# Kernel optimization log

Hardware: AMD Instinct MI355X
Metric: run time of the kernel (lower is better)

The kernel has to match this reference:

```python
import jax, jax.numpy as jnp
import numpy as np
from jax import lax

B, T = 512, 128
V, D, H, MLP, C = 50000, 300, 512, 1024, 3


def setup_inputs() -> dict:
    key = jax.random.key(0)
    ks = jax.random.split(key, 12)
    s = 0.02
    x = jax.random.randint(ks[0], (B, T), 0, V, dtype=jnp.int64)
    lengths = jax.random.randint(ks[1], (B,), 1, T + 1, dtype=jnp.int64)
    return {
        "x": x,
        "lengths": lengths,
        "E": jax.random.normal(ks[2], (V, D), jnp.float32) * s,
        "W_ih": jax.random.normal(ks[3], (H, D), jnp.float32) * s,
        "b_ih": jnp.zeros((H,), jnp.float32),
        "W_hh": jax.random.normal(ks[4], (H, H), jnp.float32) * s,
        "b_hh": jnp.zeros((H,), jnp.float32),
        "l0_w": jax.random.normal(ks[5], (MLP, H), jnp.float32) * s,
        "l0_b": jnp.zeros((MLP,), jnp.float32),
        "l1_w": jax.random.normal(ks[6], (C, MLP), jnp.float32) * s,
        "l1_b": jnp.zeros((C,), jnp.float32),
    }


def reference(x, lengths, E, W_ih, b_ih, W_hh, b_hh, l0_w, l0_b, l1_w, l1_b):
    # Original pops tokens from the end of each sample, right-aligned by length:
    # at step t the active samples (l >= T - t) consume token x[i, T-1-t],
    # i.e. each sequence is processed in reverse token order; hidden state of
    # inactive samples stays untouched (zeros until the sample becomes active).
    Bn, Tn = x.shape
    Hn = W_hh.shape[0]
    toks = x[:, ::-1].T                                    # [T, B] token at step t
    idxs = jnp.arange(Tn)[::-1]                            # index T-1-t at step t
    active = idxs[:, None] < lengths[None, :]              # [T, B]

    def step(h, inp):
        tok, m = inp
        emb = E[tok]                                       # [B, D] gather
        h_next = jnp.tanh(emb @ W_ih.T + b_ih + h @ W_hh.T + b_hh)
        h = jnp.where(m[:, None], h_next, h)               # scatter-back for active rows
        return h, None

    h0 = jnp.zeros((Bn, Hn), E.dtype)
    h, _ = lax.scan(step, h0, (toks, active))
    # eval mode: dropout(p=0.5, training=False) is identity
    a = jax.nn.relu(h @ l0_w.T + l0_b)
    logits = jax.nn.relu(a @ l1_w.T + l1_b)
    return jax.nn.log_softmax(logits, axis=-1)
```

## Files before the change

kernel.cpp:

```cpp
#include <hip/hip_runtime.h>
#include <hip/hip_bf16.h>
#include <cstdint>

#define BB 512
#define TT 128
#define VV 50000
#define DD 300
#define HH 512
#define MLPD 1024
#define CC 3

typedef __bf16 bf16x8 __attribute__((ext_vector_type(8)));
typedef float  f32x4  __attribute__((ext_vector_type(4)));
typedef float  f32x2  __attribute__((ext_vector_type(2)));
typedef int    v8i    __attribute__((ext_vector_type(8)));
typedef int    v4i    __attribute__((ext_vector_type(4)));

struct alignas(8)  bf4 { __bf16 x, y, z, w; };

__device__ __forceinline__ f32x2 tanh16pk(float x0, float x1) {
    f32x2 t;
    t.x = __builtin_amdgcn_fmed3f(x0, -0.7f, 0.7f);
    t.y = __builtin_amdgcn_fmed3f(x1, -0.7f, 0.7f);
    f32x2 u = t * t;
    f32x2 inner = u * 2.1333333f - 5.3333333f;
    return (t * u) * inner + t * 16.0f;
}

#define SCALE_H 0x7B7B7B7B
#define SCALE_W 0x7C7C7C7C

__global__ __launch_bounds__(256) void k_prep(
    const float* __restrict__ Whh, unsigned char* __restrict__ out8,
    const float* __restrict__ Wihf, __bf16* __restrict__ outih,
    const float* __restrict__ l0w, __bf16* __restrict__ outl0)
{
    if (blockIdx.x < 32) {
        const int T = blockIdx.x * 256 + threadIdx.x;
        const int lane = T & 63;
        const int kch = (T >> 6) & 3;
        const int ct  = (T >> 8) & 3;
        const int w   = (T >> 10) & 7;
        const int n = lane & 15, q = lane >> 4;
        const int c  = w * 64 + ct * 16 + n;
        const int k0 = kch * 128 + q * 32;
        const float* src = Whh + c * HH + k0;
        unsigned int wd[8];
        #pragma unroll
        for (int i = 0; i < 8; ++i) {
            float4 v = *(const float4*)(src + i * 4);
            unsigned int t0 = __builtin_amdgcn_cvt_pk_fp8_f32(v.x * 8.f, v.y * 8.f, 0, false);
            t0 = __builtin_amdgcn_cvt_pk_fp8_f32(v.z * 8.f, v.w * 8.f, t0, true);
            wd[i] = t0;
        }
        *(uint4*)(out8 + (size_t)T * 32)      = make_uint4(wd[0], wd[1], wd[2], wd[3]);
        *(uint4*)(out8 + (size_t)T * 32 + 16) = make_uint4(wd[4], wd[5], wd[6], wd[7]);
    } else if (blockIdx.x < 112) {
        const int U = (blockIdx.x - 32) * 256 + threadIdx.x;
        const int lane = U & 63;
        const int rest = U >> 6;
        const int kc = rest % 10;
        const int g  = rest / 10;
        const int c = g * 16 + (lane & 15);
        const int k = kc * 32 + (lane >> 4) * 8;
        bf16x8 o;
        #pragma unroll
        for (int j = 0; j < 8; ++j) {
            const int kk = k + j;
            o[j] = (__bf16)((kk < DD) ? Wihf[c * DD + kk] : 0.f);
        }
        *(bf16x8*)(outih + (size_t)U * 8) = o;
    } else {
        const int F = (blockIdx.x - 112) * 256 + threadIdx.x;
        const int lane = F & 63;
        const int kc = (F >> 6) & 15;
        const int nt = F >> 10;
        const int c = nt * 16 + (lane & 15);
        const int k = kc * 32 + (lane >> 4) * 8;
        const float* src = l0w + (size_t)c * HH + k;
        float4 v0 = *(const float4*)src;
        float4 v1 = *(const float4*)(src + 4);
        bf16x8 o;
        o[0]=(__bf16)v0.x; o[1]=(__bf16)v0.y; o[2]=(__bf16)v0.z; o[3]=(__bf16)v0.w;
        o[4]=(__bf16)v1.x; o[5]=(__bf16)v1.y; o[6]=(__bf16)v1.z; o[7]=(__bf16)v1.w;
        *(bf16x8*)(outl0 + (size_t)F * 8) = o;
    }
}

__global__ __launch_bounds__(256, 1) void k_proj(
    const int* __restrict__ x, const int* __restrict__ lengths,
    const float* __restrict__ E, const __bf16* __restrict__ Wih,
    const float* __restrict__ b_ih, const float* __restrict__ b_hh,
    __bf16* __restrict__ P_c)
{
    __shared__ __bf16 Afs[4][10 * 64 * 8];
    __shared__ float bias_s[HH];

    const int tq  = blockIdx.x;
    const int i0  = blockIdx.y * 64;
    const int wg0 = blockIdx.y * 4;
    const int tid = threadIdx.x;
    const int wv = tid >> 6, lane = tid & 63;
    const int np = lane & 15;

    bias_s[tid]       = b_ih[tid]       + b_hh[tid];
    bias_s[tid + 256] = b_ih[tid + 256] + b_hh[tid + 256];
    __syncthreads();

    bf16x8 Af[4][10];
    {
        const int k0a = lane * 4;
        const int cha = k0a >> 5, ga = (k0a >> 3) & 3;
        const int k0b = 256 + lane * 4;
        const int chb = k0b >> 5, gb = (k0b >> 3) & 3;
        for (int tt = 0; tt < 4; ++tt) {
            const int thr = TT - 1 - (tq * 4 + tt);
            #pragma unroll 4
            for (int rl = 0; rl < 16; ++rl) {
                const int gr = i0 + wv * 16 + rl;
                const bool act = thr < lengths[gr];
                float4 v0 = make_float4(0.f, 0.f, 0.f, 0.f);
                float4 v1 = make_float4(0.f, 0.f, 0.f, 0.f);
                if (act) {
                    const float* erow = E + (size_t)x[gr * TT + thr] * DD;
                    v0 = *(const float4*)(erow + k0a);
                    if (lane < 11) v1 = *(const float4*)(erow + k0b);
                }
                bf4 p0 = {(__bf16)v0.x, (__bf16)v0.y, (__bf16)v0.z, (__bf16)v0.w};
                *(bf4*)(&Afs[wv][((cha * 64) + rl + 16 * ga) * 8 + (k0a & 7)]) = p0;
                if (lane < 16) {
                    bf4 p1 = {(__bf16)v1.x, (__bf16)v1.y, (__bf16)v1.z, (__bf16)v1.w};
                    *(bf4*)(&Afs[wv][((chb * 64) + rl + 16 * gb) * 8 + (k0b & 7)]) = p1;
                }
            }
            #pragma unroll
            for (int kc = 0; kc < 10; ++kc)
                Af[tt][kc] = *(const bf16x8*)(&Afs[wv][(kc * 64 + lane) * 8]);
        }
    }

    for (int ntq = 0; ntq < 8; ++ntq) {
        bf4 pkbuf[4][4];
        #pragma unroll
        for (int j = 0; j < 4; ++j) {
            const int nt = ntq * 4 + j;
            const __bf16* bbase = Wih + ((size_t)(nt * 10) * 64 + lane) * 8;
            bf16x8 Bf[10];
            #pragma unroll
            for (int kc = 0; kc < 10; ++kc)
                Bf[kc] = *(const bf16x8*)(bbase + (size_t)kc * 512);

            f32x4 acc[4] = {};
            #pragma unroll
            for (int kc = 0; kc < 10; ++kc) {
                acc[0] = __builtin_amdgcn_mfma_f32_16x16x32_bf16(Af[0][kc], Bf[kc], acc[0], 0, 0, 0);
                acc[1] = __builtin_amdgcn_mfma_f32_16x16x32_bf16(Af[1][kc], Bf[kc], acc[1], 0, 0, 0);
                acc[2] = __builtin_amdgcn_mfma_f32_16x16x32_bf16(Af[2][kc], Bf[kc], acc[2], 0, 0, 0);
                acc[3] = __builtin_amdgcn_mfma_f32_16x16x32_bf16(Af[3][kc], Bf[kc], acc[3], 0, 0, 0);
            }

            const float bias = bias_s[nt * 16 + np];
            #pragma unroll
            for (int tt = 0; tt < 4; ++tt)
                pkbuf[tt][j] = bf4{(__bf16)(acc[tt][0] + bias), (__bf16)(acc[tt][1] + bias),
                                   (__bf16)(acc[tt][2] + bias), (__bf16)(acc[tt][3] + bias)};
        }
        #pragma unroll
        for (int tt = 0; tt < 4; ++tt) {
            const int t = tq * 4 + tt;
            unsigned char* dst = (unsigned char*)P_c
                + ((size_t)((t * 32 + wg0 + wv) * 8 + ntq)) * 2048 + (size_t)lane * 32;
            *(uint4*)(dst)      = *(uint4*)(&pkbuf[tt][0]);
            *(uint4*)(dst + 16) = *(uint4*)(&pkbuf[tt][2]);
        }
    }
}

#define LKH 520

__global__ __launch_bounds__(512, 2) void k_rnn(
    const int* __restrict__ lengths, const unsigned char* __restrict__ Wb8,
    const __bf16* __restrict__ P_c, const __bf16* __restrict__ l0wf,
    const float* __restrict__ l0_b, const float* __restrict__ l1_w,
    const float* __restrict__ l1_b, float* __restrict__ out)
{
    __shared__ unsigned char smem[50944];
    unsigned char (*Hs8)[8192] = (unsigned char (*)[8192])smem;
    __bf16* As   = (__bf16*)(smem + 16384);
    float*  l1s  = (float*)(smem + 33024);
    float*  l0bs = (float*)(smem + 45312);
    float (*red)[16][3] = (float (*)[16][3])(smem + 49408);

    const int tid = threadIdx.x;
    const int wg  = blockIdx.x;
    const int r0  = wg * 16;
    const int w    = tid >> 6;
    const int lane = tid & 63;
    const int n = lane & 15, q = lane >> 4;

    for (int i = tid * 16; i < 16384; i += 512 * 16)
        *(uint4*)(&smem[i]) = make_uint4(0u, 0u, 0u, 0u);

    for (int i = tid; i < 3 * MLPD; i += 512) l1s[i] = l1_w[i];
    for (int i = tid; i < MLPD; i += 512)     l0bs[i] = l0_b[i];

    const int len_n = lengths[r0 + n];
    const int tact  = TT - len_n;
    int ml = len_n;
    #pragma unroll
    for (int off = 1; off <= 8; off <<= 1) {
        int o = __shfl_xor(ml, off, 64);
        ml = ml > o ? ml : o;
    }
    const int t0 = (TT - ml) & ~1;

    v8i Wv[4][4];
    #pragma unroll
    for (int ct = 0; ct < 4; ++ct)
        #pragma unroll
        for (int kch = 0; kch < 4; ++kch)
            Wv[ct][kch] = *(const v8i*)(Wb8 + ((size_t)(((w * 4 + ct) * 4 + kch) * 64 + lane)) * 32);

    const int wsw = ((n >> 2) & 1) << 4;
    int waddr[4];
    #pragma unroll
    for (int ct = 0; ct < 4; ++ct)
        waddr[ct] = ((((w >> 1) * 64 + n + 16 * ((2 * w + (ct >> 1)) & 3)) * 32
                  + (ct & 1) * 16 + q * 4)) ^ wsw;

    const int rsw = ((lane >> 2) & 1) << 4;

    const size_t pstep = (size_t)32 * 8 * 2048;
    const unsigned char* pptr = (const unsigned char*)P_c
                              + ((size_t)(wg * 8 + w)) * 2048 + (size_t)lane * 32
                              + (size_t)t0 * pstep;

    __syncthreads();

    bf16x8 plo = *(const bf16x8*)(pptr);
    bf16x8 phi = *(const bf16x8*)(pptr + 16);
    pptr += pstep;

    auto step = [&](int t, const unsigned char* rbuf, unsigned char* wbuf) {
        bf16x8 nlo = *(const bf16x8*)(pptr);
        bf16x8 nhi = *(const bf16x8*)(pptr + 16);
        pptr += pstep;

        v8i hf[4];
        #pragma unroll
        for (int kch = 0; kch < 4; ++kch) {
            const unsigned char* rb = rbuf + (kch * 64 + lane) * 32;
            v4i lo = *(const v4i*)(rb + rsw);
            v4i hi = *(const v4i*)(rb + (16 ^ rsw));
            hf[kch] = __builtin_shufflevector(lo, hi, 0, 1, 2, 3, 4, 5, 6, 7);
        }

        const bool act = (t >= tact);

        {
            f32x4 a0, a1;
            #pragma unroll
            for (int r = 0; r < 4; ++r) { a0[r] = (float)plo[r]; a1[r] = (float)plo[4 + r]; }
            a0 = __builtin_amdgcn_mfma_scale_f32_16x16x128_f8f6f4(Wv[0][0], hf[0], a0, 0, 0, 0, SCALE_W, 0, SCALE_H);
            a1 = __builtin_amdgcn_mfma_scale_f32_16x16x128_f8f6f4(Wv[1][0], hf[0], a1, 0, 0, 0, SCALE_W, 0, SCALE_H);
            a0 = __builtin_amdgcn_mfma_scale_f32_16x16x128_f8f6f4(Wv[0][1], hf[1], a0, 0, 0, 0, SCALE_W, 0, SCALE_H);
            a1 = __builtin_amdgcn_mfma_scale_f32_16x16x128_f8f6f4(Wv[1][1], hf[1], a1, 0, 0, 0, SCALE_W, 0, SCALE_H);
            a0 = __builtin_amdgcn_mfma_scale_f32_16x16x128_f8f6f4(Wv[0][2], hf[2], a0, 0, 0, 0, SCALE_W, 0, SCALE_H);
            a1 = __builtin_amdgcn_mfma_scale_f32_16x16x128_f8f6f4(Wv[1][2], hf[2], a1, 0, 0, 0, SCALE_W, 0, SCALE_H);
            a0 = __builtin_amdgcn_mfma_scale_f32_16x16x128_f8f6f4(Wv[0][3], hf[3], a0, 0, 0, 0, SCALE_W, 0, SCALE_H);
            a1 = __builtin_amdgcn_mfma_scale_f32_16x16x128_f8f6f4(Wv[1][3], hf[3], a1, 0, 0, 0, SCALE_W, 0, SCALE_H);

            f32x2 s00 = tanh16pk(a0[0], a0[1]);
            f32x2 s01 = tanh16pk(a0[2], a0[3]);
            f32x2 s10 = tanh16pk(a1[0], a1[1]);
            f32x2 s11 = tanh16pk(a1[2], a1[3]);
            unsigned p0 = __builtin_amdgcn_cvt_pk_fp8_f32(s00.x, s00.y, 0u, false);
            p0 = __builtin_amdgcn_cvt_pk_fp8_f32(s01.x, s01.y, p0, true);
            unsigned p1 = __builtin_amdgcn_cvt_pk_fp8_f32(s10.x, s10.y, 0u, false);
            p1 = __builtin_amdgcn_cvt_pk_fp8_f32(s11.x, s11.y, p1, true);
            *(unsigned int*)(&wbuf[waddr[0]]) = act ? p0 : 0u;
            *(unsigned int*)(&wbuf[waddr[1]]) = act ? p1 : 0u;
        }

        {
            f32x4 a2, a3;
            #pragma unroll
            for (int r = 0; r < 4; ++r) { a2[r] = (float)phi[r]; a3[r] = (float)phi[4 + r]; }
            a2 = __builtin_amdgcn_mfma_scale_f32_16x16x128_f8f6f4(Wv[2][0], hf[0], a2, 0, 0, 0, SCALE_W, 0, SCALE_H);
            a3 = __builtin_amdgcn_mfma_scale_f32_16x16x128_f8f6f4(Wv[3][0], hf[0], a3, 0, 0, 0, SCALE_W, 0, SCALE_H);
            a2 = __builtin_amdgcn_mfma_scale_f32_16x16x128_f8f6f4(Wv[2][1], hf[1], a2, 0, 0, 0, SCALE_W, 0, SCALE_H);
            a3 = __builtin_amdgcn_mfma_scale_f32_16x16x128_f8f6f4(Wv[3][1], hf[1], a3, 0, 0, 0, SCALE_W, 0, SCALE_H);
            a2 = __builtin_amdgcn_mfma_scale_f32_16x16x128_f8f6f4(Wv[2][2], hf[2], a2, 0, 0, 0, SCALE_W, 0, SCALE_H);
            a3 = __builtin_amdgcn_mfma_scale_f32_16x16x128_f8f6f4(Wv[3][2], hf[2], a3, 0, 0, 0, SCALE_W, 0, SCALE_H);
            a2 = __builtin_amdgcn_mfma_scale_f32_16x16x128_f8f6f4(Wv[2][3], hf[3], a2, 0, 0, 0, SCALE_W, 0, SCALE_H);
            a3 = __builtin_amdgcn_mfma_scale_f32_16x16x128_f8f6f4(Wv[3][3], hf[3], a3, 0, 0, 0, SCALE_W, 0, SCALE_H);

            f32x2 s20 = tanh16pk(a2[0], a2[1]);
            f32x2 s21 = tanh16pk(a2[2], a2[3]);
            f32x2 s30 = tanh16pk(a3[0], a3[1]);
            f32x2 s31 = tanh16pk(a3[2], a3[3]);
            unsigned p2 = __builtin_amdgcn_cvt_pk_fp8_f32(s20.x, s20.y, 0u, false);
            p2 = __builtin_amdgcn_cvt_pk_fp8_f32(s21.x, s21.y, p2, true);
            unsigned p3 = __builtin_amdgcn_cvt_pk_fp8_f32(s30.x, s30.y, 0u, false);
            p3 = __builtin_amdgcn_cvt_pk_fp8_f32(s31.x, s31.y, p3, true);
            *(unsigned int*)(&wbuf[waddr[2]]) = act ? p2 : 0u;
            *(unsigned int*)(&wbuf[waddr[3]]) = act ? p3 : 0u;
        }

        plo = nlo; phi = nhi;
        __syncthreads();
    };

    for (int t = t0; t < TT; t += 2) {
        step(t,     Hs8[0], Hs8[1]);
        step(t + 1, Hs8[1], Hs8[0]);
    }

    {
        const int half   = tid & 1;
        const int lane_t = (tid >> 1) & 63;
        const int kch    = tid >> 7;
        const int m  = lane_t & 15, qq = lane_t >> 4;
        const int cb = kch * 128 + qq * 32 + half * 16;
        const int sw2 = ((lane_t >> 2) & 1) << 4;
        uint4 wv4 = *(const uint4*)(&Hs8[0][(kch * 64 + lane_t) * 32 + ((half * 16) ^ sw2)]);
        unsigned int ws4[4] = {wv4.x, wv4.y, wv4.z, wv4.w};
        bf16x8 o0, o1;
        #pragma unroll
        for (int wd = 0; wd < 4; ++wd) {
            float f0 = __builtin_amdgcn_cvt_f32_fp8(ws4[wd], 0) * 0.0625f;
            float f1 = __builtin_amdgcn_cvt_f32_fp8(ws4[wd], 1) * 0.0625f;
            float f2 = __builtin_amdgcn_cvt_f32_fp8(ws4[wd], 2) * 0.0625f;
            float f3 = __builtin_amdgcn_cvt_f32_fp8(ws4[wd], 3) * 0.0625f;
            if (wd < 2) {
                o0[wd * 4 + 0] = (__bf16)f0; o0[wd * 4 + 1] = (__bf16)f1;
                o0[wd * 4 + 2] = (__bf16)f2; o0[wd * 4 + 3] = (__bf16)f3;
            } else {
                o1[(wd - 2) * 4 + 0] = (__bf16)f0; o1[(wd - 2) * 4 + 1] = (__bf16)f1;
                o1[(wd - 2) * 4 + 2] = (__bf16)f2; o1[(wd - 2) * 4 + 3] = (__bf16)f3;
            }
        }
        *(bf16x8*)(&As[m * LKH + cb])     = o0;
        *(bf16x8*)(&As[m * LKH + cb + 8]) = o1;
    }
    __syncthreads();

    float pl[4][3] = {};
    for (int j = 0; j < 8; ++j) {
        const int ntile = w * 8 + j;
        const __bf16* bb = l0wf + ((size_t)(ntile * 16) * 64 + lane) * 8;
        bf16x8 Bf[16];
        #pragma unroll
        for (int kc = 0; kc < 16; ++kc)
            Bf[kc] = *(const bf16x8*)(bb + (size_t)kc * 512);

        f32x4 acc = {};
        #pragma unroll
        for (int kc = 0; kc < 16; ++kc) {
            bf16x8 a = *(const bf16x8*)(&As[n * LKH + kc * 32 + q * 8]);
            acc = __builtin_amdgcn_mfma_f32_16x16x32_bf16(a, Bf[kc], acc, 0, 0, 0);
        }

        const int col = ntile * 16 + n;
        const float b0 = l0bs[col];
        const float w0 = l1s[col], w1 = l1s[MLPD + col], w2 = l1s[2 * MLPD + col];
        #pragma unroll
        for (int r = 0; r < 4; ++r) {
            const float av = fmaxf(acc[r] + b0, 0.f);
            pl[r][0] = fmaf(av, w0, pl[r][0]);
            pl[r][1] = fmaf(av, w1, pl[r][1]);
            pl[r][2] = fmaf(av, w2, pl[r][2]);
        }
    }

    #pragma unroll
    for (int off = 1; off <= 8; off <<= 1)
        #pragma unroll
        for (int r = 0; r < 4; ++r)
            #pragma unroll
            for (int c = 0; c < 3; ++c)
                pl[r][c] += __shfl_xor(pl[r][c], off, 64);

    if (n == 0)
        #pragma unroll
        for (int r = 0; r < 4; ++r)
            #pragma unroll
            for (int c = 0; c < 3; ++c)
                red[w][q * 4 + r][c] = pl[r][c];
    __syncthreads();

    if (tid < 16) {
        const int row = tid;
        float l[3];
        #pragma unroll
        for (int c = 0; c < 3; ++c) {
            float s = l1_b[c];
            #pragma unroll
            for (int ww = 0; ww < 8; ++ww) s += red[ww][row][c];
            l[c] = fmaxf(s, 0.f);
        }
        float m = fmaxf(l[0], fmaxf(l[1], l[2]));
        float sum = expf(l[0] - m) + expf(l[1] - m) + expf(l[2] - m);
        float ls = m + logf(sum);
        out[(r0 + row) * CC + 0] = l[0] - ls;
        out[(r0 + row) * CC + 1] = l[1] - ls;
        out[(r0 + row) * CC + 2] = l[2] - ls;
    }
}

extern "C" void kernel_launch(void* const* d_in, const int* in_sizes, int n_in,
                              void* d_out, int out_size, void* d_ws, size_t ws_size,
                              hipStream_t stream) {
    const int*   x    = (const int*)  d_in[0];
    const int*   len  = (const int*)  d_in[1];
    const float* E    = (const float*)d_in[2];
    const float* W_ih = (const float*)d_in[3];
    const float* b_ih = (const float*)d_in[4];
    const float* W_hh = (const float*)d_in[5];
    const float* b_hh = (const float*)d_in[6];
    const float* l0_w = (const float*)d_in[7];
    const float* l0_b = (const float*)d_in[8];
    const float* l1_w = (const float*)d_in[9];
    const float* l1_b = (const float*)d_in[10];
    float* out = (float*)d_out;

    char* ws = (char*)d_ws;
    unsigned char* Wb8 = (unsigned char*)ws;
    __bf16* Wih   = (__bf16*)(ws + 524288);
    __bf16* l0wf  = (__bf16*)(ws + 1048576);
    __bf16* P_c   = (__bf16*)(ws + 4194304);

    k_prep<<<368, 256, 0, stream>>>(W_hh, Wb8, W_ih, Wih, l0_w, l0wf);
    dim3 g1(32, 8);
    k_proj<<<g1, 256, 0, stream>>>(x, len, E, Wih, b_ih, b_hh, P_c);
    k_rnn<<<32, 512, 0, stream>>>(len, Wb8, P_c, l0wf, l0_b, l1_w, l1_b, out);
}
```

Baseline: 323.0 us.

## Replace per-step block barrier with LDS flag-based wave sync and 4-deep ring

Each RNN time step ended in a __syncthreads. That is now replaced by per-wave progress flags in shared memory, and the hidden state moves to a 4-slot LDS ring. Each wave spins only on the flags of the two waves that produced the K-chunk it needs next. Waves start on different chunks to stagger their waits, so MFMAs on ready chunks can begin before all waves finish. In exchange the code adds busy-wait polling, more LDS use (which may affect the 2-blocks-per-CU occupancy), and memory-ordering risk from relying on lgkmcnt plus volatile flags.

```diff
diff --git a/kernel.cpp b/kernel.cpp
--- a/kernel.cpp
+++ b/kernel.cpp
@@ -184,12 +184,15 @@
     const float* __restrict__ l0_b, const float* __restrict__ l1_w,
     const float* __restrict__ l1_b, float* __restrict__ out)
 {
-    __shared__ unsigned char smem[50944];
-    unsigned char (*Hs8)[8192] = (unsigned char (*)[8192])smem;
-    __bf16* As   = (__bf16*)(smem + 16384);
-    float*  l1s  = (float*)(smem + 33024);
-    float*  l0bs = (float*)(smem + 45312);
-    float (*red)[16][3] = (float (*)[16][3])(smem + 49408);
+    __shared__ unsigned char smem[67360];
+    unsigned char* ring = smem;
+    int*    flg  = (int*)(smem + 32768);
+    __bf16* As   = (__bf16*)(smem + 32832);
+    float*  l1s  = (float*)(smem + 49472);
+    float*  l0bs = (float*)(smem + 61760);
+    float (*red)[16][3] = (float (*)[16][3])(smem + 65856);
+
+    volatile int* vflg = (volatile int*)flg;
 
     const int tid = threadIdx.x;
     const int wg  = blockIdx.x;
@@ -197,8 +200,9 @@
     const int w    = tid >> 6;
     const int lane = tid & 63;
     const int n = lane & 15, q = lane >> 4;
-
-    for (int i = tid * 16; i < 16384; i += 512 * 16)
+    const int pr = w >> 1;
+
+    for (int i = tid * 16; i < 32768; i += 512 * 16)
         *(uint4*)(&smem[i]) = make_uint4(0u, 0u, 0u, 0u);
 
     for (int i = tid; i < 3 * MLPD; i += 512) l1s[i] = l1_w[i];
@@ -212,7 +216,9 @@
         int o = __shfl_xor(ml, off, 64);
         ml = ml > o ? ml : o;
     }
-    const int t0 = (TT - ml) & ~1;
+    const int t0 = TT - ml;
+
+    if (tid < 8) flg[tid] = t0 - 1;
 
     v8i Wv[4][4];
     #pragma unroll
@@ -241,89 +247,77 @@
     bf16x8 phi = *(const bf16x8*)(pptr + 16);
     pptr += pstep;
 
-    auto step = [&](int t, const unsigned char* rbuf, unsigned char* wbuf) {
+    for (int t = t0; t < TT; ++t) {
+        const unsigned char* rbuf = ring + (size_t)((t + 3) & 3) * 8192;
+        unsigned char*       wbuf = ring + (size_t)(t & 3) * 8192;
+
         bf16x8 nlo = *(const bf16x8*)(pptr);
         bf16x8 nhi = *(const bf16x8*)(pptr + 16);
         pptr += pstep;
 
-        v8i hf[4];
-        #pragma unroll
-        for (int kch = 0; kch < 4; ++kch) {
-            const unsigned char* rb = rbuf + (kch * 64 + lane) * 32;
+        const bool act = (t >= tact);
+        const int tm1 = t - 1;
+
+        f32x4 a0, a1, a2, a3;
+        #pragma unroll
+        for (int r = 0; r < 4; ++r) {
+            a0[r] = (float)plo[r]; a1[r] = (float)plo[4 + r];
+            a2[r] = (float)phi[r]; a3[r] = (float)phi[4 + r];
+        }
+
+        #pragma unroll
+        for (int g = 0; g < 4; ++g) {
+            const int kk = (pr + g) & 3;
+            while (vflg[2 * kk] < tm1 || vflg[2 * kk + 1] < tm1) {}
+            asm volatile("" ::: "memory");
+            const unsigned char* rb = rbuf + (kk * 64 + lane) * 32;
             v4i lo = *(const v4i*)(rb + rsw);
             v4i hi = *(const v4i*)(rb + (16 ^ rsw));
-            hf[kch] = __builtin_shufflevector(lo, hi, 0, 1, 2, 3, 4, 5, 6, 7);
-        }
-
-        const bool act = (t >= tact);
-
-        {
-            f32x4 a0, a1;
-            #pragma unroll
-            for (int r = 0; r < 4; ++r) { a0[r] = (float)plo[r]; a1[r] = (float)plo[4 + r]; }
-            a0 = __builtin_amdgcn_mfma_scale_f32_16x16x128_f8f6f4(Wv[0][0], hf[0], a0, 0, 0, 0, SCALE_W, 0, SCALE_H);
-            a1 = __builtin_amdgcn_mfma_scale_f32_16x16x128_f8f6f4(Wv[1][0], hf[0], a1, 0, 0, 0, SCALE_W, 0, SCALE_H);
-            a0 = __builtin_amdgcn_mfma_scale_f32_16x16x128_f8f6f4(Wv[0][1], hf[1], a0, 0, 0, 0, SCALE_W, 0, SCALE_H);
-            a1 = __builtin_amdgcn_mfma_scale_f32_16x16x128_f8f6f4(Wv[1][1], hf[1], a1, 0, 0, 0, SCALE_W, 0, SCALE_H);
-            a0 = __builtin_amdgcn_mfma_scale_f32_16x16x128_f8f6f4(Wv[0][2], hf[2], a0, 0, 0, 0, SCALE_W, 0, SCALE_H);
-            a1 = __builtin_amdgcn_mfma_scale_f32_16x16x128_f8f6f4(Wv[1][2], hf[2], a1, 0, 0, 0, SCALE_W, 0, SCALE_H);
-            a0 = __builtin_amdgcn_mfma_scale_f32_16x16x128_f8f6f4(Wv[0][3], hf[3], a0, 0, 0, 0, SCALE_W, 0, SCALE_H);
-            a1 = __builtin_amdgcn_mfma_scale_f32_16x16x128_f8f6f4(Wv[1][3], hf[3], a1, 0, 0, 0, SCALE_W, 0, SCALE_H);
-
-            f32x2 s00 = tanh16pk(a0[0], a0[1]);
-            f32x2 s01 = tanh16pk(a0[2], a0[3]);
-            f32x2 s10 = tanh16pk(a1[0], a1[1]);
-            f32x2 s11 = tanh16pk(a1[2], a1[3]);
-            unsigned p0 = __builtin_amdgcn_cvt_pk_fp8_f32(s00.x, s00.y, 0u, false);
-            p0 = __builtin_amdgcn_cvt_pk_fp8_f32(s01.x, s01.y, p0, true);
-            unsigned p1 = __builtin_amdgcn_cvt_pk_fp8_f32(s10.x, s10.y, 0u, false);
-            p1 = __builtin_amdgcn_cvt_pk_fp8_f32(s11.x, s11.y, p1, true);
-            *(unsigned int*)(&wbuf[waddr[0]]) = act ? p0 : 0u;
-            *(unsigned int*)(&wbuf[waddr[1]]) = act ? p1 : 0u;
-        }
-
-        {
-            f32x4 a2, a3;
-            #pragma unroll
-            for (int r = 0; r < 4; ++r) { a2[r] = (float)phi[r]; a3[r] = (float)phi[4 + r]; }
-            a2 = __builtin_amdgcn_mfma_scale_f32_16x16x128_f8f6f4(Wv[2][0], hf[0], a2, 0, 0, 0, SCALE_W, 0, SCALE_H);
-            a3 = __builtin_amdgcn_mfma_scale_f32_16x16x128_f8f6f4(Wv[3][0], hf[0], a3, 0, 0, 0, SCALE_W, 0, SCALE_H);
-            a2 = __builtin_amdgcn_mfma_scale_f32_16x16x128_f8f6f4(Wv[2][1], hf[1], a2, 0, 0, 0, SCALE_W, 0, SCALE_H);
-            a3 = __builtin_amdgcn_mfma_scale_f32_16x16x128_f8f6f4(Wv[3][1], hf[1], a3, 0, 0, 0, SCALE_W, 0, SCALE_H);
-            a2 = __builtin_amdgcn_mfma_scale_f32_16x16x128_f8f6f4(Wv[2][2], hf[2], a2, 0, 0, 0, SCALE_W, 0, SCALE_H);
-            a3 = __builtin_amdgcn_mfma_scale_f32_16x16x128_f8f6f4(Wv[3][2], hf[2], a3, 0, 0, 0, SCALE_W, 0, SCALE_H);
-            a2 = __builtin_amdgcn_mfma_scale_f32_16x16x128_f8f6f4(Wv[2][3], hf[3], a2, 0, 0, 0, SCALE_W, 0, SCALE_H);
-            a3 = __builtin_amdgcn_mfma_scale_f32_16x16x128_f8f6f4(Wv[3][3], hf[3], a3, 0, 0, 0, SCALE_W, 0, SCALE_H);
-
-            f32x2 s20 = tanh16pk(a2[0], a2[1]);
-            f32x2 s21 = tanh16pk(a2[2], a2[3]);
-            f32x2 s30 = tanh16pk(a3[0], a3[1]);
-            f32x2 s31 = tanh16pk(a3[2], a3[3]);
-            unsigned p2 = __builtin_amdgcn_cvt_pk_fp8_f32(s20.x, s20.y, 0u, false);
-            p2 = __builtin_amdgcn_cvt_pk_fp8_f32(s21.x, s21.y, p2, true);
-            unsigned p3 = __builtin_amdgcn_cvt_pk_fp8_f32(s30.x, s30.y, 0u, false);
-            p3 = __builtin_amdgcn_cvt_pk_fp8_f32(s31.x, s31.y, p3, true);
-            *(unsigned int*)(&wbuf[waddr[2]]) = act ? p2 : 0u;
-            *(unsigned int*)(&wbuf[waddr[3]]) = act ? p3 : 0u;
-        }
+            v8i hfk = __builtin_shufflevector(lo, hi, 0, 1, 2, 3, 4, 5, 6, 7);
+            a0 = __builtin_amdgcn_mfma_scale_f32_16x16x128_f8f6f4(Wv[0][kk], hfk, a0, 0, 0, 0, SCALE_W, 0, SCALE_H);
+            a1 = __builtin_amdgcn_mfma_scale_f32_16x16x128_f8f6f4(Wv[1][kk], hfk, a1, 0, 0, 0, SCALE_W, 0, SCALE_H);
+            a2 = __builtin_amdgcn_mfma_scale_f32_16x16x128_f8f6f4(Wv[2][kk], hfk, a2, 0, 0, 0, SCALE_W, 0, SCALE_H);
+            a3 = __builtin_amdgcn_mfma_scale_f32_16x16x128_f8f6f4(Wv[3][kk], hfk, a3, 0, 0, 0, SCALE_W, 0, SCALE_H);
+        }
+
+        f32x2 s00 = tanh16pk(a0[0], a0[1]);
+        f32x2 s01 = tanh16pk(a0[2], a0[3]);
+        f32x2 s10 = tanh16pk(a1[0], a1[1]);
+        f32x2 s11 = tanh16pk(a1[2], a1[3]);
+        f32x2 s20 = tanh16pk(a2[0], a2[1]);
+        f32x2 s21 = tanh16pk(a2[2], a2[3]);
+        f32x2 s30 = tanh16pk(a3[0], a3[1]);
+        f32x2 s31 = tanh16pk(a3[2], a3[3]);
+        unsigned p0 = __builtin_amdgcn_cvt_pk_fp8_f32(s00.x, s00.y, 0u, false);
+        p0 = __builtin_amdgcn_cvt_pk_fp8_f32(s01.x, s01.y, p0, true);
+        unsigned p1 = __builtin_amdgcn_cvt_pk_fp8_f32(s10.x, s10.y, 0u, false);
+        p1 = __builtin_amdgcn_cvt_pk_fp8_f32(s11.x, s11.y, p1, true);
+        unsigned p2 = __builtin_amdgcn_cvt_pk_fp8_f32(s20.x, s20.y, 0u, false);
+        p2 = __builtin_amdgcn_cvt_pk_fp8_f32(s21.x, s21.y, p2, true);
+        unsigned p3 = __builtin_amdgcn_cvt_pk_fp8_f32(s30.x, s30.y, 0u, false);
+        p3 = __builtin_amdgcn_cvt_pk_fp8_f32(s31.x, s31.y, p3, true);
+        *(unsigned int*)(&wbuf[waddr[0]]) = act ? p0 : 0u;
+        *(unsigned int*)(&wbuf[waddr[1]]) = act ? p1 : 0u;
+        *(unsigned int*)(&wbuf[waddr[2]]) = act ? p2 : 0u;
+        *(unsigned int*)(&wbuf[waddr[3]]) = act ? p3 : 0u;
+
+        asm volatile("s_waitcnt lgkmcnt(0)" ::: "memory");
+        vflg[w] = t;
 
         plo = nlo; phi = nhi;
-        __syncthreads();
-    };
-
-    for (int t = t0; t < TT; t += 2) {
-        step(t,     Hs8[0], Hs8[1]);
-        step(t + 1, Hs8[1], Hs8[0]);
-    }
+    }
+
+    __syncthreads();
 
     {
+        const unsigned char* hfin = ring + (size_t)((TT - 1) & 3) * 8192;
         const int half   = tid & 1;
         const int lane_t = (tid >> 1) & 63;
         const int kch    = tid >> 7;
         const int m  = lane_t & 15, qq = lane_t >> 4;
         const int cb = kch * 128 + qq * 32 + half * 16;
         const int sw2 = ((lane_t >> 2) & 1) << 4;
-        uint4 wv4 = *(const uint4*)(&Hs8[0][(kch * 64 + lane_t) * 32 + ((half * 16) ^ sw2)]);
+        uint4 wv4 = *(const uint4*)(&hfin[(kch * 64 + lane_t) * 32 + ((half * 16) ^ sw2)]);
         unsigned int ws4[4] = {wv4.x, wv4.y, wv4.z, wv4.w};
         bf16x8 o0, o1;
         #pragma unroll
```

Result: slower. 1.180 ms (+265.2%).

## Sort samples by length to skip inactive projection tiles and shorten RNN loops

Applied to the files above, without the earlier changes.

Adds a single-block rank sort of sequence lengths that produces a permutation and a per-64-row maximum length. The input projection gathers rows through the permutation, and whole blocks return early when every sample in the tile is inactive at those timesteps. The projection grid is doubled with two timesteps per block and occupancy 2 to keep the skip finer grained. The RNN kernel reads the permuted rows, so each 16-row group has similar lengths and can start later, and outputs are scattered back to their original rows. The cost is an extra kernel launch plus indirect loads.

```diff
diff --git a/kernel.cpp b/kernel.cpp
--- a/kernel.cpp
+++ b/kernel.cpp
@@ -29,6 +29,24 @@
 
 #define SCALE_H 0x7B7B7B7B
 #define SCALE_W 0x7C7C7C7C
+
+__global__ __launch_bounds__(512) void k_sort(
+    const int* __restrict__ lengths, int* __restrict__ perm,
+    int* __restrict__ tileMax)
+{
+    __shared__ int ls[BB];
+    const int i = threadIdx.x;
+    const int li = lengths[i];
+    ls[i] = li;
+    __syncthreads();
+    int rank = 0;
+    for (int j = 0; j < BB; ++j) {
+        const int lj = ls[j];
+        rank += (lj > li) || (lj == li && j < i);
+    }
+    perm[rank] = i;
+    if ((rank & 63) == 0) tileMax[rank >> 6] = li;
+}
 
 __global__ __launch_bounds__(256) void k_prep(
     const float* __restrict__ Whh, unsigned char* __restrict__ out8,
@@ -87,12 +105,15 @@
     }
 }
 
-__global__ __launch_bounds__(256, 1) void k_proj(
+__global__ __launch_bounds__(256, 2) void k_proj(
     const int* __restrict__ x, const int* __restrict__ lengths,
     const float* __restrict__ E, const __bf16* __restrict__ Wih,
     const float* __restrict__ b_ih, const float* __restrict__ b_hh,
-    __bf16* __restrict__ P_c)
+    __bf16* __restrict__ P_c, const int* __restrict__ perm,
+    const int* __restrict__ tileMax)
 {
+    if (tileMax[blockIdx.y] + 2 * (int)blockIdx.x < 127) return;
+
     __shared__ __bf16 Afs[4][10 * 64 * 8];
     __shared__ float bias_s[HH];
 
@@ -107,22 +128,23 @@
     bias_s[tid + 256] = b_ih[tid + 256] + b_hh[tid + 256];
     __syncthreads();
 
-    bf16x8 Af[4][10];
+    bf16x8 Af[2][10];
     {
         const int k0a = lane * 4;
         const int cha = k0a >> 5, ga = (k0a >> 3) & 3;
         const int k0b = 256 + lane * 4;
         const int chb = k0b >> 5, gb = (k0b >> 3) & 3;
-        for (int tt = 0; tt < 4; ++tt) {
-            const int thr = TT - 1 - (tq * 4 + tt);
+        for (int tt = 0; tt < 2; ++tt) {
+            const int thr = TT - 1 - (tq * 2 + tt);
             #pragma unroll 4
             for (int rl = 0; rl < 16; ++rl) {
                 const int gr = i0 + wv * 16 + rl;
-                const bool act = thr < lengths[gr];
+                const int pg = perm[gr];
+                const bool act = thr < lengths[pg];
                 float4 v0 = make_float4(0.f, 0.f, 0.f, 0.f);
                 float4 v1 = make_float4(0.f, 0.f, 0.f, 0.f);
                 if (act) {
-                    const float* erow = E + (size_t)x[gr * TT + thr] * DD;
+                    const float* erow = E + (size_t)x[pg * TT + thr] * DD;
                     v0 = *(const float4*)(erow + k0a);
                     if (lane < 11) v1 = *(const float4*)(erow + k0b);
                 }
@@ -140,7 +162,7 @@
     }
 
     for (int ntq = 0; ntq < 8; ++ntq) {
-        bf4 pkbuf[4][4];
+        bf4 pkbuf[2][4];
         #pragma unroll
         for (int j = 0; j < 4; ++j) {
             const int nt = ntq * 4 + j;
@@ -150,24 +172,22 @@
             for (int kc = 0; kc < 10; ++kc)
                 Bf[kc] = *(const bf16x8*)(bbase + (size_t)kc * 512);
 
-            f32x4 acc[4] = {};
+            f32x4 acc[2] = {};
             #pragma unroll
             for (int kc = 0; kc < 10; ++kc) {
                 acc[0] = __builtin_amdgcn_mfma_f32_16x16x32_bf16(Af[0][kc], Bf[kc], acc[0], 0, 0, 0);
                 acc[1] = __builtin_amdgcn_mfma_f32_16x16x32_bf16(Af[1][kc], Bf[kc], acc[1], 0, 0, 0);
-                acc[2] = __builtin_amdgcn_mfma_f32_16x16x32_bf16(Af[2][kc], Bf[kc], acc[2], 0, 0, 0);
-                acc[3] = __builtin_amdgcn_mfma_f32_16x16x32_bf16(Af[3][kc], Bf[kc], acc[3], 0, 0, 0);
             }
 
             const float bias = bias_s[nt * 16 + np];
             #pragma unroll
-            for (int tt = 0; tt < 4; ++tt)
+            for (int tt = 0; tt < 2; ++tt)
                 pkbuf[tt][j] = bf4{(__bf16)(acc[tt][0] + bias), (__bf16)(acc[tt][1] + bias),
                                    (__bf16)(acc[tt][2] + bias), (__bf16)(acc[tt][3] + bias)};
         }
         #pragma unroll
-        for (int tt = 0; tt < 4; ++tt) {
-            const int t = tq * 4 + tt;
+        for (int tt = 0; tt < 2; ++tt) {
+            const int t = tq * 2 + tt;
             unsigned char* dst = (unsigned char*)P_c
                 + ((size_t)((t * 32 + wg0 + wv) * 8 + ntq)) * 2048 + (size_t)lane * 32;
             *(uint4*)(dst)      = *(uint4*)(&pkbuf[tt][0]);
@@ -182,7 +202,8 @@
     const int* __restrict__ lengths, const unsigned char* __restrict__ Wb8,
     const __bf16* __restrict__ P_c, const __bf16* __restrict__ l0wf,
     const float* __restrict__ l0_b, const float* __restrict__ l1_w,
-    const float* __restrict__ l1_b, float* __restrict__ out)
+    const float* __restrict__ l1_b, float* __restrict__ out,
+    const int* __restrict__ perm)
 {
     __shared__ unsigned char smem[50944];
     unsigned char (*Hs8)[8192] = (unsigned char (*)[8192])smem;
@@ -204,7 +225,7 @@
     for (int i = tid; i < 3 * MLPD; i += 512) l1s[i] = l1_w[i];
     for (int i = tid; i < MLPD; i += 512)     l0bs[i] = l0_b[i];
 
-    const int len_n = lengths[r0 + n];
+    const int len_n = lengths[perm[r0 + n]];
     const int tact  = TT - len_n;
     int ml = len_n;
     #pragma unroll
@@ -391,6 +412,7 @@
 
     if (tid < 16) {
         const int row = tid;
+        const int orow = perm[r0 + row];
         float l[3];
         #pragma unroll
         for (int c = 0; c < 3; ++c) {
@@ -402,9 +424,9 @@
         float m = fmaxf(l[0], fmaxf(l[1], l[2]));
         float sum = expf(l[0] - m) + expf(l[1] - m) + expf(l[2] - m);
         float ls = m + logf(sum);
-        out[(r0 + row) * CC + 0] = l[0] - ls;
-        out[(r0 + row) * CC + 1] = l[1] - ls;
-        out[(r0 + row) * CC + 2] = l[2] - ls;
+        out[orow * CC + 0] = l[0] - ls;
+        out[orow * CC + 1] = l[1] - ls;
+        out[orow * CC + 2] = l[2] - ls;
     }
 }
 
@@ -428,10 +450,13 @@
     unsigned char* Wb8 = (unsigned char*)ws;
     __bf16* Wih   = (__bf16*)(ws + 524288);
     __bf16* l0wf  = (__bf16*)(ws + 1048576);
+    int* permW    = (int*)(ws + 2097152);
+    int* tileMaxW = (int*)(ws + 2097152 + 2048);
     __bf16* P_c   = (__bf16*)(ws + 4194304);
 
     k_prep<<<368, 256, 0, stream>>>(W_hh, Wb8, W_ih, Wih, l0_w, l0wf);
-    dim3 g1(32, 8);
-    k_proj<<<g1, 256, 0, stream>>>(x, len, E, Wih, b_ih, b_hh, P_c);
-    k_rnn<<<32, 512, 0, stream>>>(len, Wb8, P_c, l0wf, l0_b, l1_w, l1_b, out);
-}
+    k_sort<<<1, 512, 0, stream>>>(len, permW, tileMaxW);
+    dim3 g1(64, 8);
+    k_proj<<<g1, 256, 0, stream>>>(x, len, E, Wih, b_ih, b_hh, P_c, permW, tileMaxW);
+    k_rnn<<<32, 512, 0, stream>>>(len, Wb8, P_c, l0wf, l0_b, l1_w, l1_b, out, permW);
+}
```

New measurement: 314.5 us. 1.03x faster.

## Halve RNN block to 4 waves with 8 column tiles each; split projection over more blocks

Applied to the files above, without the earlier changes.

The recurrent kernel now runs 256 threads (4 waves) per block instead of 8 waves. Each wave holds twice as many W_hh fp8 fragments in registers and issues 8 independent MFMA chains per k-chunk, so fewer waves meet at each per-step barrier and each wave has more instruction-level parallelism. The projection kernel processes 2 timesteps per block over a 64x8 grid, with launch bounds raised to 2 blocks per CU for more parallelism. The cost is much higher register pressure in k_rnn, which could spill, plus halved wave-level parallelism in the serial loop and the MLP epilogue.

```diff
diff --git a/kernel.cpp b/kernel.cpp
--- a/kernel.cpp
+++ b/kernel.cpp
@@ -87,7 +87,7 @@
     }
 }
 
-__global__ __launch_bounds__(256, 1) void k_proj(
+__global__ __launch_bounds__(256, 2) void k_proj(
     const int* __restrict__ x, const int* __restrict__ lengths,
     const float* __restrict__ E, const __bf16* __restrict__ Wih,
     const float* __restrict__ b_ih, const float* __restrict__ b_hh,
@@ -107,14 +107,14 @@
     bias_s[tid + 256] = b_ih[tid + 256] + b_hh[tid + 256];
     __syncthreads();
 
-    bf16x8 Af[4][10];
+    bf16x8 Af[2][10];
     {
         const int k0a = lane * 4;
         const int cha = k0a >> 5, ga = (k0a >> 3) & 3;
         const int k0b = 256 + lane * 4;
         const int chb = k0b >> 5, gb = (k0b >> 3) & 3;
-        for (int tt = 0; tt < 4; ++tt) {
-            const int thr = TT - 1 - (tq * 4 + tt);
+        for (int tt = 0; tt < 2; ++tt) {
+            const int thr = TT - 1 - (tq * 2 + tt);
             #pragma unroll 4
             for (int rl = 0; rl < 16; ++rl) {
                 const int gr = i0 + wv * 16 + rl;
@@ -140,7 +140,7 @@
     }
 
     for (int ntq = 0; ntq < 8; ++ntq) {
-        bf4 pkbuf[4][4];
+        bf4 pkbuf[2][4];
         #pragma unroll
         for (int j = 0; j < 4; ++j) {
             const int nt = ntq * 4 + j;
@@ -150,24 +150,22 @@
             for (int kc = 0; kc < 10; ++kc)
                 Bf[kc] = *(const bf16x8*)(bbase + (size_t)kc * 512);
 
-            f32x4 acc[4] = {};
+            f32x4 acc[2] = {};
             #pragma unroll
             for (int kc = 0; kc < 10; ++kc) {
                 acc[0] = __builtin_amdgcn_mfma_f32_16x16x32_bf16(Af[0][kc], Bf[kc], acc[0], 0, 0, 0);
                 acc[1] = __builtin_amdgcn_mfma_f32_16x16x32_bf16(Af[1][kc], Bf[kc], acc[1], 0, 0, 0);
-                acc[2] = __builtin_amdgcn_mfma_f32_16x16x32_bf16(Af[2][kc], Bf[kc], acc[2], 0, 0, 0);
-                acc[3] = __builtin_amdgcn_mfma_f32_16x16x32_bf16(Af[3][kc], Bf[kc], acc[3], 0, 0, 0);
             }
 
             const float bias = bias_s[nt * 16 + np];
             #pragma unroll
-            for (int tt = 0; tt < 4; ++tt)
+            for (int tt = 0; tt < 2; ++tt)
                 pkbuf[tt][j] = bf4{(__bf16)(acc[tt][0] + bias), (__bf16)(acc[tt][1] + bias),
                                    (__bf16)(acc[tt][2] + bias), (__bf16)(acc[tt][3] + bias)};
         }
         #pragma unroll
-        for (int tt = 0; tt < 4; ++tt) {
-            const int t = tq * 4 + tt;
+        for (int tt = 0; tt < 2; ++tt) {
+            const int t = tq * 2 + tt;
             unsigned char* dst = (unsigned char*)P_c
                 + ((size_t)((t * 32 + wg0 + wv) * 8 + ntq)) * 2048 + (size_t)lane * 32;
             *(uint4*)(dst)      = *(uint4*)(&pkbuf[tt][0]);
@@ -178,7 +176,7 @@
 
 #define LKH 520
 
-__global__ __launch_bounds__(512, 2) void k_rnn(
+__global__ __launch_bounds__(256, 1) void k_rnn(
     const int* __restrict__ lengths, const unsigned char* __restrict__ Wb8,
     const __bf16* __restrict__ P_c, const __bf16* __restrict__ l0wf,
     const float* __restrict__ l0_b, const float* __restrict__ l1_w,
@@ -198,11 +196,11 @@
     const int lane = tid & 63;
     const int n = lane & 15, q = lane >> 4;
 
-    for (int i = tid * 16; i < 16384; i += 512 * 16)
+    for (int i = tid * 16; i < 16384; i += 256 * 16)
         *(uint4*)(&smem[i]) = make_uint4(0u, 0u, 0u, 0u);
 
-    for (int i = tid; i < 3 * MLPD; i += 512) l1s[i] = l1_w[i];
-    for (int i = tid; i < MLPD; i += 512)     l0bs[i] = l0_b[i];
+    for (int i = tid; i < 3 * MLPD; i += 256) l1s[i] = l1_w[i];
+    for (int i = tid; i < MLPD; i += 256)     l0bs[i] = l0_b[i];
 
     const int len_n = lengths[r0 + n];
     const int tact  = TT - len_n;
@@ -214,36 +212,39 @@
     }
     const int t0 = (TT - ml) & ~1;
 
-    v8i Wv[4][4];
+    v8i Wv[8][4];
     #pragma unroll
-    for (int ct = 0; ct < 4; ++ct)
+    for (int j = 0; j < 8; ++j)
         #pragma unroll
         for (int kch = 0; kch < 4; ++kch)
-            Wv[ct][kch] = *(const v8i*)(Wb8 + ((size_t)(((w * 4 + ct) * 4 + kch) * 64 + lane)) * 32);
+            Wv[j][kch] = *(const v8i*)(Wb8 + ((size_t)(((w * 8 + j) * 4 + kch) * 64 + lane)) * 32);
 
     const int wsw = ((n >> 2) & 1) << 4;
-    int waddr[4];
+    int waddr[8];
     #pragma unroll
-    for (int ct = 0; ct < 4; ++ct)
-        waddr[ct] = ((((w >> 1) * 64 + n + 16 * ((2 * w + (ct >> 1)) & 3)) * 32
-                  + (ct & 1) * 16 + q * 4)) ^ wsw;
+    for (int j = 0; j < 8; ++j)
+        waddr[j] = ((w * 64 + n + 16 * (j >> 1)) * 32 + (j & 1) * 16 + q * 4) ^ wsw;
 
     const int rsw = ((lane >> 2) & 1) << 4;
 
     const size_t pstep = (size_t)32 * 8 * 2048;
     const unsigned char* pptr = (const unsigned char*)P_c
-                              + ((size_t)(wg * 8 + w)) * 2048 + (size_t)lane * 32
+                              + ((size_t)(wg * 8 + 2 * w)) * 2048 + (size_t)lane * 32
                               + (size_t)t0 * pstep;
 
     __syncthreads();
 
-    bf16x8 plo = *(const bf16x8*)(pptr);
-    bf16x8 phi = *(const bf16x8*)(pptr + 16);
+    bf16x8 p0lo = *(const bf16x8*)(pptr);
+    bf16x8 p0hi = *(const bf16x8*)(pptr + 16);
+    bf16x8 p1lo = *(const bf16x8*)(pptr + 2048);
+    bf16x8 p1hi = *(const bf16x8*)(pptr + 2064);
     pptr += pstep;
 
     auto step = [&](int t, const unsigned char* rbuf, unsigned char* wbuf) {
-        bf16x8 nlo = *(const bf16x8*)(pptr);
-        bf16x8 nhi = *(const bf16x8*)(pptr + 16);
+        bf16x8 n0lo = *(const bf16x8*)(pptr);
+        bf16x8 n0hi = *(const bf16x8*)(pptr + 16);
+        bf16x8 n1lo = *(const bf16x8*)(pptr + 2048);
+        bf16x8 n1hi = *(const bf16x8*)(pptr + 2064);
         pptr += pstep;
 
         v8i hf[4];
@@ -257,57 +258,37 @@
 
         const bool act = (t >= tact);
 
-        {
-            f32x4 a0, a1;
-            #pragma unroll
-            for (int r = 0; r < 4; ++r) { a0[r] = (float)plo[r]; a1[r] = (float)plo[4 + r]; }
-            a0 = __builtin_amdgcn_mfma_scale_f32_16x16x128_f8f6f4(Wv[0][0], hf[0], a0, 0, 0, 0, SCALE_W, 0, SCALE_H);
-            a1 = __builtin_amdgcn_mfma_scale_f32_16x16x128_f8f6f4(Wv[1][0], hf[0], a1, 0, 0, 0, SCALE_W, 0, SCALE_H);
-            a0 = __builtin_amdgcn_mfma_scale_f32_16x16x128_f8f6f4(Wv[0][1], hf[1], a0, 0, 0, 0, SCALE_W, 0, SCALE_H);
-            a1 = __builtin_amdgcn_mfma_scale_f32_16x16x128_f8f6f4(Wv[1][1], hf[1], a1, 0, 0, 0, SCALE_W, 0, SCALE_H);
-            a0 = __builtin_amdgcn_mfma_scale_f32_16x16x128_f8f6f4(Wv[0][2], hf[2], a0, 0, 0, 0, SCALE_W, 0, SCALE_H);
-            a1 = __builtin_amdgcn_mfma_scale_f32_16x16x128_f8f6f4(Wv[1][2], hf[2], a1, 0, 0, 0, SCALE_W, 0, SCALE_H);
-            a0 = __builtin_amdgcn_mfma_scale_f32_16x16x128_f8f6f4(Wv[0][3], hf[3], a0, 0, 0, 0, SCALE_W, 0, SCALE_H);
-            a1 = __builtin_amdgcn_mfma_scale_f32_16x16x128_f8f6f4(Wv[1][3], hf[3], a1, 0, 0, 0, SCALE_W, 0, SCALE_H);
-
-            f32x2 s00 = tanh16pk(a0[0], a0[1]);
-            f32x2 s01 = tanh16pk(a0[2], a0[3]);
-            f32x2 s10 = tanh16pk(a1[0], a1[1]);
-            f32x2 s11 = tanh16pk(a1[2], a1[3]);
-            unsigned p0 = __builtin_amdgcn_cvt_pk_fp8_f32(s00.x, s00.y, 0u, false);
-            p0 = __builtin_amdgcn_cvt_pk_fp8_f32(s01.x, s01.y, p0, true);
-            unsigned p1 = __builtin_amdgcn_cvt_pk_fp8_f32(s10.x, s10.y, 0u, false);
-            p1 = __builtin_amdgcn_cvt_pk_fp8_f32(s11.x, s11.y, p1, true);
-            *(unsigned int*)(&wbuf[waddr[0]]) = act ? p0 : 0u;
-            *(unsigned int*)(&wbuf[waddr[1]]) = act ? p1 : 0u;
-        }
-
-        {
-            f32x4 a2, a3;
-            #pragma unroll
-            for (int r = 0; r < 4; ++r) { a2[r] = (float)phi[r]; a3[r] = (float)phi[4 + r]; }
-            a2 = __builtin_amdgcn_mfma_scale_f32_16x16x128_f8f6f4(Wv[2][0], hf[0], a2, 0, 0, 0, SCALE_W, 0, SCALE_H);
-            a3 = __builtin_amdgcn_mfma_scale_f32_16x16x128_f8f6f4(Wv[3][0], hf[0], a3, 0, 0, 0, SCALE_W, 0, SCALE_H);
-            a2 = __builtin_amdgcn_mfma_scale_f32_16x16x128_f8f6f4(Wv[2][1], hf[1], a2, 0, 0, 0, SCALE_W, 0, SCALE_H);
-            a3 = __builtin_amdgcn_mfma_scale_f32_16x16x128_f8f6f4(Wv[3][1], hf[1], a3, 0, 0, 0, SCALE_W, 0, SCALE_H);
-            a2 = __builtin_amdgcn_mfma_scale_f32_16x16x128_f8f6f4(Wv[2][2], hf[2], a2, 0, 0, 0, SCALE_W, 0, SCALE_H);
-            a3 = __builtin_amdgcn_mfma_scale_f32_16x16x128_f8f6f4(Wv[3][2], hf[2], a3, 0, 0, 0, SCALE_W, 0, SCALE_H);
-            a2 = __builtin_amdgcn_mfma_scale_f32_16x16x128_f8f6f4(Wv[2][3], hf[3], a2, 0, 0, 0, SCALE_W, 0, SCALE_H);
-            a3 = __builtin_amdgcn_mfma_scale_f32_16x16x128_f8f6f4(Wv[3][3], hf[3], a3, 0, 0, 0, SCALE_W, 0, SCALE_H);
-
-            f32x2 s20 = tanh16pk(a2[0], a2[1]);
-            f32x2 s21 = tanh16pk(a2[2], a2[3]);
-            f32x2 s30 = tanh16pk(a3[0], a3[1]);
-            f32x2 s31 = tanh16pk(a3[2], a3[3]);
-            unsigned p2 = __builtin_amdgcn_cvt_pk_fp8_f32(s20.x, s20.y, 0u, false);
-            p2 = __builtin_amdgcn_cvt_pk_fp8_f32(s21.x, s21.y, p2, true);
-            unsigned p3 = __builtin_amdgcn_cvt_pk_fp8_f32(s30.x, s30.y, 0u, false);
-            p3 = __builtin_amdgcn_cvt_pk_fp8_f32(s31.x, s31.y, p3, true);
-            *(unsigned int*)(&wbuf[waddr[2]]) = act ? p2 : 0u;
-            *(unsigned int*)(&wbuf[waddr[3]]) = act ? p3 : 0u;
-        }
-
-        plo = nlo; phi = nhi;
+        f32x4 a[8];
+        #pragma unroll
+        for (int r = 0; r < 4; ++r) {
+            a[0][r] = (float)p0lo[r];     a[1][r] = (float)p0lo[4 + r];
+            a[2][r] = (float)p0hi[r];     a[3][r] = (float)p0hi[4 + r];
+            a[4][r] = (float)p1lo[r];     a[5][r] = (float)p1lo[4 + r];
+            a[6][r] = (float)p1hi[r];     a[7][r] = (float)p1hi[4 + r];
+        }
+
+        #pragma unroll
+        for (int kch = 0; kch < 4; ++kch) {
+            a[0] = __builtin_amdgcn_mfma_scale_f32_16x16x128_f8f6f4(Wv[0][kch], hf[kch], a[0], 0, 0, 0, SCALE_W, 0, SCALE_H);
+            a[1] = __builtin_amdgcn_mfma_scale_f32_16x16x128_f8f6f4(Wv[1][kch], hf[kch], a[1], 0, 0, 0, SCALE_W, 0, SCALE_H);
+            a[2] = __builtin_amdgcn_mfma_scale_f32_16x16x128_f8f6f4(Wv[2][kch], hf[kch], a[2], 0, 0, 0, SCALE_W, 0, SCALE_H);
+            a[3] = __builtin_amdgcn_mfma_scale_f32_16x16x128_f8f6f4(Wv[3][kch], hf[kch], a[3], 0, 0, 0, SCALE_W, 0, SCALE_H);
+            a[4] = __builtin_amdgcn_mfma_scale_f32_16x16x128_f8f6f4(Wv[4][kch], hf[kch], a[4], 0, 0, 0, SCALE_W, 0, SCALE_H);
+            a[5] = __builtin_amdgcn_mfma_scale_f32_16x16x128_f8f6f4(Wv[5][kch], hf[kch], a[5], 0, 0, 0, SCALE_W, 0, SCALE_H);
+            a[6] = __builtin_amdgcn_mfma_scale_f32_16x16x128_f8f6f4(Wv[6][kch], hf[kch], a[6], 0, 0, 0, SCALE_W, 0, SCALE_H);
+            a[7] = __builtin_amdgcn_mfma_scale_f32_16x16x128_f8f6f4(Wv[7][kch], hf[kch], a[7], 0, 0, 0, SCALE_W, 0, SCALE_H);
+        }
+
+        #pragma unroll
+        for (int j = 0; j < 8; ++j) {
+            f32x2 sA = tanh16pk(a[j][0], a[j][1]);
+            f32x2 sB = tanh16pk(a[j][2], a[j][3]);
+            unsigned pk = __builtin_amdgcn_cvt_pk_fp8_f32(sA.x, sA.y, 0u, false);
+            pk = __builtin_amdgcn_cvt_pk_fp8_f32(sB.x, sB.y, pk, true);
+            *(unsigned int*)(&wbuf[waddr[j]]) = act ? pk : 0u;
+        }
+
+        p0lo = n0lo; p0hi = n0hi; p1lo = n1lo; p1hi = n1hi;
         __syncthreads();
     };
 
@@ -319,35 +300,39 @@
     {
         const int half   = tid & 1;
         const int lane_t = (tid >> 1) & 63;
-        const int kch    = tid >> 7;
+        const int kb     = tid >> 7;
         const int m  = lane_t & 15, qq = lane_t >> 4;
-        const int cb = kch * 128 + qq * 32 + half * 16;
         const int sw2 = ((lane_t >> 2) & 1) << 4;
-        uint4 wv4 = *(const uint4*)(&Hs8[0][(kch * 64 + lane_t) * 32 + ((half * 16) ^ sw2)]);
-        unsigned int ws4[4] = {wv4.x, wv4.y, wv4.z, wv4.w};
-        bf16x8 o0, o1;
-        #pragma unroll
-        for (int wd = 0; wd < 4; ++wd) {
-            float f0 = __builtin_amdgcn_cvt_f32_fp8(ws4[wd], 0) * 0.0625f;
-            float f1 = __builtin_amdgcn_cvt_f32_fp8(ws4[wd], 1) * 0.0625f;
-            float f2 = __builtin_amdgcn_cvt_f32_fp8(ws4[wd], 2) * 0.0625f;
-            float f3 = __builtin_amdgcn_cvt_f32_fp8(ws4[wd], 3) * 0.0625f;
-            if (wd < 2) {
-                o0[wd * 4 + 0] = (__bf16)f0; o0[wd * 4 + 1] = (__bf16)f1;
-                o0[wd * 4 + 2] = (__bf16)f2; o0[wd * 4 + 3] = (__bf16)f3;
-            } else {
-                o1[(wd - 2) * 4 + 0] = (__bf16)f0; o1[(wd - 2) * 4 + 1] = (__bf16)f1;
-                o1[(wd - 2) * 4 + 2] = (__bf16)f2; o1[(wd - 2) * 4 + 3] = (__bf16)f3;
+        #pragma unroll
+        for (int it = 0; it < 2; ++it) {
+            const int kch = kb * 2 + it;
+            const int cb = kch * 128 + qq * 32 + half * 16;
+            uint4 wv4 = *(const uint4*)(&Hs8[0][(kch * 64 + lane_t) * 32 + ((half * 16) ^ sw2)]);
+            unsigned int ws4[4] = {wv4.x, wv4.y, wv4.z, wv4.w};
+            bf16x8 o0, o1;
+            #pragma unroll
+            for (int wd = 0; wd < 4; ++wd) {
+                float f0 = __builtin_amdgcn_cvt_f32_fp8(ws4[wd], 0) * 0.0625f;
+                float f1 = __builtin_amdgcn_cvt_f32_fp8(ws4[wd], 1) * 0.0625f;
+                float f2 = __builtin_amdgcn_cvt_f32_fp8(ws4[wd], 2) * 0.0625f;
+                float f3 = __builtin_amdgcn_cvt_f32_fp8(ws4[wd], 3) * 0.0625f;
+                if (wd < 2) {
+                    o0[wd * 4 + 0] = (__bf16)f0; o0[wd * 4 + 1] = (__bf16)f1;
+                    o0[wd * 4 + 2] = (__bf16)f2; o0[wd * 4 + 3] = (__bf16)f3;
+                } else {
+                    o1[(wd - 2) * 4 + 0] = (__bf16)f0; o1[(wd - 2) * 4 + 1] = (__bf16)f1;
+                    o1[(wd - 2) * 4 + 2] = (__bf16)f2; o1[(wd - 2) * 4 + 3] = (__bf16)f3;
+                }
             }
-        }
-        *(bf16x8*)(&As[m * LKH + cb])     = o0;
-        *(bf16x8*)(&As[m * LKH + cb + 8]) = o1;
+            *(bf16x8*)(&As[m * LKH + cb])     = o0;
+            *(bf16x8*)(&As[m * LKH + cb + 8]) = o1;
+        }
     }
     __syncthreads();
 
     float pl[4][3] = {};
-    for (int j = 0; j < 8; ++j) {
-        const int ntile = w * 8 + j;
+    for (int j = 0; j < 16; ++j) {
+        const int ntile = w * 16 + j;
         const __bf16* bb = l0wf + ((size_t)(ntile * 16) * 64 + lane) * 8;
         bf16x8 Bf[16];
         #pragma unroll
@@ -396,7 +381,7 @@
         for (int c = 0; c < 3; ++c) {
             float s = l1_b[c];
             #pragma unroll
-            for (int ww = 0; ww < 8; ++ww) s += red[ww][row][c];
+            for (int ww = 0; ww < 4; ++ww) s += red[ww][row][c];
             l[c] = fmaxf(s, 0.f);
         }
         float m = fmaxf(l[0], fmaxf(l[1], l[2]));
@@ -431,7 +416,7 @@
     __bf16* P_c   = (__bf16*)(ws + 4194304);
 
     k_prep<<<368, 256, 0, stream>>>(W_hh, Wb8, W_ih, Wih, l0_w, l0wf);
-    dim3 g1(32, 8);
+    dim3 g1(64, 8);
     k_proj<<<g1, 256, 0, stream>>>(x, len, E, Wih, b_ih, b_hh, P_c);
-    k_rnn<<<32, 512, 0, stream>>>(len, Wb8, P_c, l0wf, l0_b, l1_w, l1_b, out);
+    k_rnn<<<32, 256, 0, stream>>>(len, Wb8, P_c, l0wf, l0_b, l1_w, l1_b, out);
 }
```

Result: slower. 333.9 us (+3.4%).
